# Optimization experiments

Measured on AMD Instinct MI355X. Metric: run time of the kernel, lower is better.

The kernel has to match this reference:

```python
import jax, jax.numpy as jnp
import numpy as np

F_CH = 12   # self.f
R = 2       # self.r
LN_EPS = 1e-5


def setup_inputs() -> dict:
    key = jax.random.key(0)
    ks = jax.random.split(key, 12)
    B, C, h, w = 1024, 200, 15, 15
    f, fr = F_CH, F_CH // R
    X = jax.random.normal(ks[0], (B, C, h, w), dtype=jnp.float32)
    # 1x1 conv weights stored as [out, in]; biases [out]
    s_in = 1.0 / np.sqrt(C)
    w11 = jax.random.normal(ks[1], (f, C), dtype=jnp.float32) * s_in
    b11 = jax.random.normal(ks[2], (f,), dtype=jnp.float32) * 0.01
    w21 = jax.random.normal(ks[3], (f, C), dtype=jnp.float32) * s_in
    b21 = jax.random.normal(ks[4], (f,), dtype=jnp.float32) * 0.01
    w31 = jax.random.normal(ks[5], (f, C), dtype=jnp.float32) * s_in
    b31 = jax.random.normal(ks[6], (f,), dtype=jnp.float32) * 0.01
    w41 = jax.random.normal(ks[7], (fr, f), dtype=jnp.float32) * (1.0 / np.sqrt(f))
    b41 = jax.random.normal(ks[8], (fr,), dtype=jnp.float32) * 0.01
    w42 = jax.random.normal(ks[9], (C, fr), dtype=jnp.float32) * (1.0 / np.sqrt(fr))
    b42 = jax.random.normal(ks[10], (C,), dtype=jnp.float32) * 0.01
    ln_g = jnp.ones((C,), dtype=jnp.float32)
    ln_b = jnp.zeros((C,), dtype=jnp.float32)
    return {"X": X, "w11": w11, "b11": b11, "w21": w21, "b21": b21,
            "w31": w31, "b31": b31, "w41": w41, "b41": b41,
            "w42": w42, "b42": b42, "ln_g": ln_g, "ln_b": ln_b}


def reference(X, w11, b11, w21, b21, w31, b31, w41, b41, w42, b42, ln_g, ln_b):
    B, C, h, w = X.shape
    f = F_CH
    HW = h * w
    Xf = X.reshape(B, C, HW)                       # flatten spatial for 1x1 convs
    k = jnp.einsum('bcn,fc->bfn', Xf, w11) + b11[:, None]   # [B,f,HW]
    q = jnp.einsum('bcn,fc->bfn', Xf, w21) + b21[:, None]
    kq = k * q                                               # [B,f,HW]
    v = jnp.einsum('bcn,fc->bfn', Xf, w31) + b31[:, None]    # [B,f,HW]
    # original: permute to [B,h,w,f] then raw reshape to [B,f,1,HW] (scrambles data)
    vp = jnp.transpose(v.reshape(B, f, h, w), (0, 2, 3, 1)).reshape(B, f, HW)
    vm = jnp.mean(vp, axis=-1)                               # adaptive avg pool -> [B,f]
    vs = jax.nn.softmax(vm, axis=1)                          # nn.Softmax default dim=1 on 4D
    # einsum 'bkij,blik->bijl' with i=1: out[b,j,l] = (sum_k kq[b,k,j]) * vs[b,l]
    kqs = jnp.sum(kq, axis=1)                                # [B,HW]
    x41 = kqs[:, :, None] * vs[:, None, :]                   # [B,HW,f]
    x = x41 @ w41.T + b41                                    # conv41: [B,HW,f//r]
    x = x @ w42.T + b42                                      # conv42: [B,HW,C]
    mu = jnp.mean(x, axis=-1, keepdims=True)
    var = jnp.var(x, axis=-1, keepdims=True)
    xn = (x - mu) / jnp.sqrt(var + LN_EPS) * ln_g + ln_b     # LayerNorm(C)
    x42 = jax.nn.sigmoid(jax.nn.relu(xn))                    # [B,HW,C]
    gate = jnp.transpose(x42, (0, 2, 1)).reshape(B, C, h, w)
    return gate * X
```

## Files before the change

### kernel.cpp

```cpp
#include <hip/hip_runtime.h>
#include <math.h>

#define F_CH 12
#define C_DIM 200
#define HW 225
#define PERB (C_DIM*HW)
#define LN_EPS 1e-5f

#define WS_WT   0
#define WS_DP   7200
#define WS_VARD 7400

__global__ __launch_bounds__(256) void k_prep(
    const float* __restrict__ w11, const float* __restrict__ w21,
    const float* __restrict__ w31, const float* __restrict__ b41,
    const float* __restrict__ w42, const float* __restrict__ b42,
    float* __restrict__ wT, float* __restrict__ Dp, float* __restrict__ varD)
{
    const int tid = threadIdx.x;
    for (int i = tid; i < 36*C_DIM; i += 256) {
        int c = i / 36, g = i - 36*c;
        float v;
        if (g < 12)      v = w11[g*C_DIM + c];
        else if (g < 24) v = w21[(g-12)*C_DIM + c];
        else             v = w31[(g-24)*C_DIM + c];
        wT[i] = v;
    }
    __shared__ float red[12];
    __shared__ float DmSh;
    float d = 0.f;
    if (tid < C_DIM) {
        float s = b42[tid];
#pragma unroll
        for (int j = 0; j < 6; ++j) s = fmaf(w42[tid*6+j], b41[j], s);
        d = s;
    }
    float s0 = d;
    for (int o = 32; o > 0; o >>= 1) s0 += __shfl_down(s0, o, 64);
    if ((tid & 63) == 0) red[tid >> 6] = s0;
    __syncthreads();
    if (tid == 0) DmSh = (red[0]+red[1]+red[2]+red[3]) * (1.f/C_DIM);
    __syncthreads();
    float dp = (tid < C_DIM) ? (d - DmSh) : 0.f;
    if (tid < C_DIM) Dp[tid] = dp;
    float s1 = dp*dp;
    for (int o = 32; o > 0; o >>= 1) s1 += __shfl_down(s1, o, 64);
    if ((tid & 63) == 0) red[4 + (tid >> 6)] = s1;
    __syncthreads();
    if (tid == 0) varD[0] = (red[4]+red[5]+red[6]+red[7]) * (1.f/C_DIM);
}

__global__ __launch_bounds__(256, 4) void k_fused(
    const float* __restrict__ X,
    const float* __restrict__ wT,
    const float* __restrict__ b11, const float* __restrict__ b21,
    const float* __restrict__ b31,
    const float* __restrict__ w41,
    const float* __restrict__ w42,
    const float* __restrict__ Dp, const float* __restrict__ varDp,
    const float* __restrict__ ln_g, const float* __restrict__ ln_b,
    float* __restrict__ out)
{
    const int b   = blockIdx.x;
    const int tid = threadIdx.x;

    __shared__ float vmb[F_CH];
    __shared__ float vsS[F_CH];
    __shared__ float t1S[6];
    __shared__ float red[12];
    __shared__ float AmSh, varASh, covSh;
    __shared__ float AgS[C_DIM], DgS[C_DIM], blS[C_DIM];

    const float varD = varDp[0];

    float accK[F_CH], accQ[F_CH], accV[F_CH];
#pragma unroll
    for (int f = 0; f < F_CH; ++f) { accK[f] = b11[f]; accQ[f] = b21[f]; accV[f] = b31[f]; }

    const int n = (tid < HW) ? tid : (HW-1);
    const float* xcol = X + (size_t)b*PERB + n;

#define CONV_STEP(CBASE, XR)                                              \
    {                                                                     \
        const float* wr_ = wT + (CBASE)*36;                               \
        _Pragma("unroll")                                                 \
        for (int u = 0; u < 4; ++u) {                                     \
            float xv_ = XR[u];                                            \
            const float* wu_ = wr_ + u*36;                                \
            _Pragma("unroll")                                             \
            for (int f = 0; f < F_CH; ++f) {                              \
                accK[f] = fmaf(xv_, wu_[f],    accK[f]);                  \
                accQ[f] = fmaf(xv_, wu_[12+f], accQ[f]);                  \
                accV[f] = fmaf(xv_, wu_[24+f], accV[f]);                  \
            }                                                             \
        }                                                                 \
    }

    float xA[4], xB[4];
#pragma unroll
    for (int u = 0; u < 4; ++u) xA[u] = xcol[(size_t)u*HW];
#pragma unroll
    for (int u = 0; u < 4; ++u) xB[u] = xcol[(size_t)(4+u)*HW];
    for (int c = 0; c < C_DIM - 8; c += 4) {
        float xC[4];
        const float* xn4 = xcol + (size_t)(c+8)*HW;
#pragma unroll
        for (int u = 0; u < 4; ++u) xC[u] = xn4[(size_t)u*HW];
        CONV_STEP(c, xA);
#pragma unroll
        for (int u = 0; u < 4; ++u) { xA[u] = xB[u]; xB[u] = xC[u]; }
    }
    CONV_STEP(C_DIM-8, xA);
    CONV_STEP(C_DIM-4, xB);
#undef CONV_STEP

    float kq = 0.f;
#pragma unroll
    for (int f = 0; f < F_CH; ++f) kq = fmaf(accK[f], accQ[f], kq);

    if (tid < F_CH) vmb[tid] = 0.f;
    __syncthreads();

    if (tid < HW) {
        int m0 = 12*tid;
        int a0 = m0/225, a1 = (m0+11)/225;
        if (a0 == a1) {
            float s = 0.f;
#pragma unroll
            for (int f = 0; f < F_CH; ++f) s += accV[f];
            atomicAdd(&vmb[a0], s);
        } else {
            int split = 225*a1 - m0;
            float sa = 0.f, sb = 0.f;
#pragma unroll
            for (int f = 0; f < F_CH; ++f) { if (f < split) sa += accV[f]; else sb += accV[f]; }
            atomicAdd(&vmb[a0], sa);
            atomicAdd(&vmb[a1], sb);
        }
    }
    __syncthreads();

    if (tid == 0) {
        float v[F_CH], mx = -1e30f;
#pragma unroll
        for (int a = 0; a < F_CH; ++a) { v[a] = vmb[a]*(1.f/HW); mx = fmaxf(mx, v[a]); }
        float s = 0.f;
#pragma unroll
        for (int a = 0; a < F_CH; ++a) { v[a] = __expf(v[a]-mx); s += v[a]; }
        float inv = 1.f/s;
#pragma unroll
        for (int a = 0; a < F_CH; ++a) vsS[a] = v[a]*inv;
    }
    __syncthreads();

    if (tid < 6) {
        float s = 0.f;
#pragma unroll
        for (int l = 0; l < F_CH; ++l) s = fmaf(w41[tid*F_CH+l], vsS[l], s);
        t1S[tid] = s;
    }
    __syncthreads();

    float A = 0.f, AD = 0.f;
    if (tid < C_DIM) {
        float s = 0.f;
#pragma unroll
        for (int j = 0; j < 6; ++j) s = fmaf(w42[tid*6+j], t1S[j], s);
        A = s;
        AD = A * Dp[tid];
    }
    float r0 = A, r1 = A*A, r2 = AD;
    for (int o = 32; o > 0; o >>= 1) {
        r0 += __shfl_down(r0, o, 64);
        r1 += __shfl_down(r1, o, 64);
        r2 += __shfl_down(r2, o, 64);
    }
    if ((tid & 63) == 0) { int w = tid>>6; red[w*3]=r0; red[w*3+1]=r1; red[w*3+2]=r2; }
    __syncthreads();
    if (tid == 0) {
        float S0 = red[0]+red[3]+red[6]+red[9];
        float S1 = red[1]+red[4]+red[7]+red[10];
        float S2 = red[2]+red[5]+red[8]+red[11];
        float Am = S0*(1.f/C_DIM);
        AmSh   = Am;
        varASh = S1*(1.f/C_DIM) - Am*Am;
        covSh  = S2*(1.f/C_DIM);
    }
    __syncthreads();

    if (tid < C_DIM) {
        float g  = ln_g[tid];
        AgS[tid] = (A - AmSh)*g;
        DgS[tid] = Dp[tid]*g;
        blS[tid] = ln_b[tid];
    }
    float Pn = 0.f, Rn = 0.f;
    if (tid < HW) {
        float var = fmaf(kq*kq, varASh, fmaf(2.f*kq, covSh, varD));
        float rs  = rsqrtf(var + LN_EPS);
        Pn = kq*rs;
        Rn = rs;
    }
    __syncthreads();

    if (tid < HW) {
        const float* __restrict__ xb = X   + (size_t)b*PERB + tid;
        float*       __restrict__ ob = out + (size_t)b*PERB + tid;
        float v0[4];
#pragma unroll
        for (int u = 0; u < 4; ++u) v0[u] = xb[(size_t)u*HW];
        for (int c = 0; c < C_DIM - 4; c += 4) {
            float nv[4];
            const float* xn4 = xb + (size_t)(c+4)*HW;
#pragma unroll
            for (int u = 0; u < 4; ++u) nv[u] = xn4[(size_t)u*HW];
#pragma unroll
            for (int u = 0; u < 4; ++u) {
                int cc = c + u;
                float xn   = fmaf(Pn, AgS[cc], fmaf(Rn, DgS[cc], blS[cc]));
                float gate = (xn > 0.f) ? (1.f/(1.f+__expf(-xn))) : 0.5f;
                __builtin_nontemporal_store(gate * v0[u], &ob[(size_t)cc*HW]);
            }
#pragma unroll
            for (int u = 0; u < 4; ++u) v0[u] = nv[u];
        }
#pragma unroll
        for (int u = 0; u < 4; ++u) {
            int cc = C_DIM - 4 + u;
            float xn   = fmaf(Pn, AgS[cc], fmaf(Rn, DgS[cc], blS[cc]));
            float gate = (xn > 0.f) ? (1.f/(1.f+__expf(-xn))) : 0.5f;
            __builtin_nontemporal_store(gate * v0[u], &ob[(size_t)cc*HW]);
        }
    }
}

extern "C" void kernel_launch(void* const* d_in, const int* in_sizes, int n_in,
                              void* d_out, int out_size, void* d_ws, size_t ws_size,
                              hipStream_t stream) {
    const float* X   = (const float*)d_in[0];
    const float* w11 = (const float*)d_in[1];
    const float* b11 = (const float*)d_in[2];
    const float* w21 = (const float*)d_in[3];
    const float* b21 = (const float*)d_in[4];
    const float* w31 = (const float*)d_in[5];
    const float* b31 = (const float*)d_in[6];
    const float* w41 = (const float*)d_in[7];
    const float* b41 = (const float*)d_in[8];
    const float* w42 = (const float*)d_in[9];
    const float* b42 = (const float*)d_in[10];
    const float* lng = (const float*)d_in[11];
    const float* lnb = (const float*)d_in[12];
    float* out = (float*)d_out;
    float* ws  = (float*)d_ws;

    float* wT = ws + WS_WT;
    float* Dp = ws + WS_DP;
    float* vD = ws + WS_VARD;

    hipLaunchKernelGGL(k_prep, dim3(1), dim3(256), 0, stream,
                       w11, w21, w31, b41, w42, b42, wT, Dp, vD);
    hipLaunchKernelGGL(k_fused, dim3(1024), dim3(256), 0, stream,
                       X, wT, b11, b21, b31, w41, w42, Dp, vD, lng, lnb, out);
}
```

Measured before the change: 385.0 us.

## Split channel reduction across two thread halves with shared-memory partial sum merge

Doubles the block to 512 threads. Each half computes the K/Q/V 1x1-conv partial sums over 100 of the 200 input channels, and the second half passes its partials to the first through a 36x226 shared-memory buffer. The final gating/store pass is also split by channel half, and the softmax and conv41 steps are merged into a single thread to remove one barrier. This is meant to shorten the serial per-thread channel loop and add memory-level parallelism, at the cost of about 33 KB of extra shared memory per block and a tighter register budget from the (512, 8) launch bounds.

```diff
diff --git a/kernel.cpp b/kernel.cpp
--- a/kernel.cpp
+++ b/kernel.cpp
@@ -3,6 +3,7 @@
 
 #define F_CH 12
 #define C_DIM 200
+#define C_HALF 100
 #define HW 225
 #define PERB (C_DIM*HW)
 #define LN_EPS 1e-5f
@@ -50,7 +51,7 @@
     if (tid == 0) varD[0] = (red[4]+red[5]+red[6]+red[7]) * (1.f/C_DIM);
 }
 
-__global__ __launch_bounds__(256, 4) void k_fused(
+__global__ __launch_bounds__(512, 8) void k_fused(
     const float* __restrict__ X,
     const float* __restrict__ wT,
     const float* __restrict__ b11, const float* __restrict__ b21,
@@ -61,28 +62,37 @@
     const float* __restrict__ ln_g, const float* __restrict__ ln_b,
     float* __restrict__ out)
 {
-    const int b   = blockIdx.x;
-    const int tid = threadIdx.x;
-
+    const int b    = blockIdx.x;
+    const int tid  = threadIdx.x;
+    const int half = tid >> 8;
+    const int lt   = tid & 255;
+
+    __shared__ float M[36*226];
+    __shared__ float PS[HW], RS[HW];
     __shared__ float vmb[F_CH];
-    __shared__ float vsS[F_CH];
     __shared__ float t1S[6];
-    __shared__ float red[12];
+    __shared__ float red[24];
     __shared__ float AmSh, varASh, covSh;
     __shared__ float AgS[C_DIM], DgS[C_DIM], blS[C_DIM];
 
     const float varD = varDp[0];
 
     float accK[F_CH], accQ[F_CH], accV[F_CH];
-#pragma unroll
-    for (int f = 0; f < F_CH; ++f) { accK[f] = b11[f]; accQ[f] = b21[f]; accV[f] = b31[f]; }
-
-    const int n = (tid < HW) ? tid : (HW-1);
-    const float* xcol = X + (size_t)b*PERB + n;
+    if (half == 0) {
+#pragma unroll
+        for (int f = 0; f < F_CH; ++f) { accK[f] = b11[f]; accQ[f] = b21[f]; accV[f] = b31[f]; }
+    } else {
+#pragma unroll
+        for (int f = 0; f < F_CH; ++f) { accK[f] = 0.f; accQ[f] = 0.f; accV[f] = 0.f; }
+    }
+
+    const int n = (lt < HW) ? lt : (HW-1);
+    const float* xcol  = X  + (size_t)b*PERB + (size_t)(half*C_HALF)*HW + n;
+    const float* wbase = wT + (size_t)(half*C_HALF)*36;
 
 #define CONV_STEP(CBASE, XR)                                              \
     {                                                                     \
-        const float* wr_ = wT + (CBASE)*36;                               \
+        const float* wr_ = wbase + (CBASE)*36;                            \
         _Pragma("unroll")                                                 \
         for (int u = 0; u < 4; ++u) {                                     \
             float xv_ = XR[u];                                            \
@@ -101,7 +111,7 @@
     for (int u = 0; u < 4; ++u) xA[u] = xcol[(size_t)u*HW];
 #pragma unroll
     for (int u = 0; u < 4; ++u) xB[u] = xcol[(size_t)(4+u)*HW];
-    for (int c = 0; c < C_DIM - 8; c += 4) {
+    for (int c = 0; c < C_HALF - 8; c += 4) {
         float xC[4];
         const float* xn4 = xcol + (size_t)(c+8)*HW;
 #pragma unroll
@@ -110,18 +120,32 @@
 #pragma unroll
         for (int u = 0; u < 4; ++u) { xA[u] = xB[u]; xB[u] = xC[u]; }
     }
-    CONV_STEP(C_DIM-8, xA);
-    CONV_STEP(C_DIM-4, xB);
+    CONV_STEP(C_HALF-8, xA);
+    CONV_STEP(C_HALF-4, xB);
 #undef CONV_STEP
 
+    if (tid < F_CH) vmb[tid] = 0.f;
+    if (half == 1 && lt < HW) {
+#pragma unroll
+        for (int f = 0; f < F_CH; ++f) {
+            M[f*226 + lt]      = accK[f];
+            M[(12+f)*226 + lt] = accQ[f];
+            M[(24+f)*226 + lt] = accV[f];
+        }
+    }
+    __syncthreads();
+
     float kq = 0.f;
-#pragma unroll
-    for (int f = 0; f < F_CH; ++f) kq = fmaf(accK[f], accQ[f], kq);
-
-    if (tid < F_CH) vmb[tid] = 0.f;
-    __syncthreads();
-
     if (tid < HW) {
+#pragma unroll
+        for (int f = 0; f < F_CH; ++f) {
+            accK[f] += M[f*226 + tid];
+            accQ[f] += M[(12+f)*226 + tid];
+            accV[f] += M[(24+f)*226 + tid];
+        }
+#pragma unroll
+        for (int f = 0; f < F_CH; ++f) kq = fmaf(accK[f], accQ[f], kq);
+
         int m0 = 12*tid;
         int a0 = m0/225, a1 = (m0+11)/225;
         if (a0 == a1) {
@@ -149,15 +173,14 @@
         for (int a = 0; a < F_CH; ++a) { v[a] = __expf(v[a]-mx); s += v[a]; }
         float inv = 1.f/s;
 #pragma unroll
-        for (int a = 0; a < F_CH; ++a) vsS[a] = v[a]*inv;
-    }
-    __syncthreads();
-
-    if (tid < 6) {
-        float s = 0.f;
-#pragma unroll
-        for (int l = 0; l < F_CH; ++l) s = fmaf(w41[tid*F_CH+l], vsS[l], s);
-        t1S[tid] = s;
+        for (int a = 0; a < F_CH; ++a) v[a] *= inv;
+#pragma unroll
+        for (int j = 0; j < 6; ++j) {
+            float t = 0.f;
+#pragma unroll
+            for (int l = 0; l < F_CH; ++l) t = fmaf(w41[j*F_CH+l], v[l], t);
+            t1S[j] = t;
+        }
     }
     __syncthreads();
 
@@ -178,9 +201,9 @@
     if ((tid & 63) == 0) { int w = tid>>6; red[w*3]=r0; red[w*3+1]=r1; red[w*3+2]=r2; }
     __syncthreads();
     if (tid == 0) {
-        float S0 = red[0]+red[3]+red[6]+red[9];
-        float S1 = red[1]+red[4]+red[7]+red[10];
-        float S2 = red[2]+red[5]+red[8]+red[11];
+        float S0 = 0.f, S1 = 0.f, S2 = 0.f;
+#pragma unroll
+        for (int w = 0; w < 8; ++w) { S0 += red[w*3]; S1 += red[w*3+1]; S2 += red[w*3+2]; }
         float Am = S0*(1.f/C_DIM);
         AmSh   = Am;
         varASh = S1*(1.f/C_DIM) - Am*Am;
@@ -194,42 +217,43 @@
         DgS[tid] = Dp[tid]*g;
         blS[tid] = ln_b[tid];
     }
-    float Pn = 0.f, Rn = 0.f;
     if (tid < HW) {
         float var = fmaf(kq*kq, varASh, fmaf(2.f*kq, covSh, varD));
         float rs  = rsqrtf(var + LN_EPS);
-        Pn = kq*rs;
-        Rn = rs;
-    }
-    __syncthreads();
-
-    if (tid < HW) {
-        const float* __restrict__ xb = X   + (size_t)b*PERB + tid;
-        float*       __restrict__ ob = out + (size_t)b*PERB + tid;
+        PS[tid] = kq*rs;
+        RS[tid] = rs;
+    }
+    __syncthreads();
+
+    if (lt < HW) {
+        float Pn = PS[lt], Rn = RS[lt];
+        const int cofs = half*C_HALF;
+        const float* __restrict__ xb = X   + (size_t)b*PERB + (size_t)cofs*HW + lt;
+        float*       __restrict__ ob = out + (size_t)b*PERB + (size_t)cofs*HW + lt;
         float v0[4];
 #pragma unroll
         for (int u = 0; u < 4; ++u) v0[u] = xb[(size_t)u*HW];
-        for (int c = 0; c < C_DIM - 4; c += 4) {
+        for (int c = 0; c < C_HALF - 4; c += 4) {
             float nv[4];
             const float* xn4 = xb + (size_t)(c+4)*HW;
 #pragma unroll
             for (int u = 0; u < 4; ++u) nv[u] = xn4[(size_t)u*HW];
 #pragma unroll
             for (int u = 0; u < 4; ++u) {
-                int cc = c + u;
+                int cc = cofs + c + u;
                 float xn   = fmaf(Pn, AgS[cc], fmaf(Rn, DgS[cc], blS[cc]));
                 float gate = (xn > 0.f) ? (1.f/(1.f+__expf(-xn))) : 0.5f;
-                __builtin_nontemporal_store(gate * v0[u], &ob[(size_t)cc*HW]);
+                __builtin_nontemporal_store(gate * v0[u], &ob[(size_t)(c+u)*HW]);
             }
 #pragma unroll
             for (int u = 0; u < 4; ++u) v0[u] = nv[u];
         }
 #pragma unroll
         for (int u = 0; u < 4; ++u) {
-            int cc = C_DIM - 4 + u;
+            int cc = cofs + C_HALF - 4 + u;
             float xn   = fmaf(Pn, AgS[cc], fmaf(Rn, DgS[cc], blS[cc]));
             float gate = (xn > 0.f) ? (1.f/(1.f+__expf(-xn))) : 0.5f;
-            __builtin_nontemporal_store(gate * v0[u], &ob[(size_t)cc*HW]);
+            __builtin_nontemporal_store(gate * v0[u], &ob[(size_t)(C_HALF-4+u)*HW]);
         }
     }
 }
@@ -259,6 +283,6 @@
 
     hipLaunchKernelGGL(k_prep, dim3(1), dim3(256), 0, stream,
                        w11, w21, w31, b41, w42, b42, wT, Dp, vD);
-    hipLaunchKernelGGL(k_fused, dim3(1024), dim3(256), 0, stream,
+    hipLaunchKernelGGL(k_fused, dim3(1024), dim3(512), 0, stream,
                        X, wT, b11, b21, b31, w41, w42, Dp, vD, lng, lnb, out);
 }
```

Result: slower. 911.1 us (+136.6%).
